# Optimization experiments

Hardware: AMD Instinct MI355X
Metric: run time of the kernel (lower is better)

## Reference

```python
import jax, jax.numpy as jnp
import numpy as np

N_NODES = 20000
N_EDGES = 320000
IN_CH = 512
HID = 128
HEADS = 4
OUT_CH = 256
NEG_SLOPE = 0.2


def _gat_layer(x, edge_index, W, a_src, a_dst, bias, heads, out_ch, concat):
    """PyG GATConv (add_self_loops=True, eval mode: no dropout).
    x: [N, F_in], edge_index: [2, E] (row 0 = src, row 1 = dst).
    Returns (out, alpha) with alpha: [E+N, heads].
    """
    N = x.shape[0]
    h = (x @ W).reshape(N, heads, out_ch)                      # [N, H, C]
    loops = jnp.arange(N, dtype=edge_index.dtype)
    src = jnp.concatenate([edge_index[0], loops])
    dst = jnp.concatenate([edge_index[1], loops])
    a_s = jnp.einsum('nhc,hc->nh', h, a_src)                   # [N, H]
    a_d = jnp.einsum('nhc,hc->nh', h, a_dst)
    e = a_s[src] + a_d[dst]                                    # [E', H]
    e = jnp.where(e > 0, e, NEG_SLOPE * e)                     # LeakyReLU
    # segment softmax over incoming edges of each dst node
    emax = jax.ops.segment_max(e, dst, num_segments=N)
    ex = jnp.exp(e - emax[dst])
    denom = jax.ops.segment_sum(ex, dst, num_segments=N)
    alpha = ex / denom[dst]                                    # [E', H]
    msg = alpha[:, :, None] * h[src]                           # [E', H, C]
    out = jax.ops.segment_sum(msg, dst, num_segments=N)        # [N, H, C]
    out = out.reshape(N, heads * out_ch) if concat else out.mean(axis=1)
    return out + bias, alpha


def setup_inputs() -> dict:
    key = jax.random.key(0)
    ks = jax.random.split(key, 10)
    s = 0.05
    x = jax.random.normal(ks[0], (N_NODES, IN_CH), dtype=jnp.float32)
    edge_index = jax.random.randint(ks[1], (2, N_EDGES), 0, N_NODES, dtype=jnp.int32)
    W1 = jax.random.normal(ks[2], (IN_CH, HEADS * HID), dtype=jnp.float32) * s
    a_src1 = jax.random.normal(ks[3], (HEADS, HID), dtype=jnp.float32) * s
    a_dst1 = jax.random.normal(ks[4], (HEADS, HID), dtype=jnp.float32) * s
    b1 = jnp.zeros((HEADS * HID,), dtype=jnp.float32)
    W2 = jax.random.normal(ks[5], (HEADS * HID, OUT_CH), dtype=jnp.float32) * s
    a_src2 = jax.random.normal(ks[6], (1, OUT_CH), dtype=jnp.float32) * s
    a_dst2 = jax.random.normal(ks[7], (1, OUT_CH), dtype=jnp.float32) * s
    b2 = jnp.zeros((OUT_CH,), dtype=jnp.float32)
    return {"x": x, "edge_index": edge_index, "W1": W1, "a_src1": a_src1,
            "a_dst1": a_dst1, "b1": b1, "W2": W2, "a_src2": a_src2,
            "a_dst2": a_dst2, "b2": b2}


def reference(x, edge_index, W1, a_src1, a_dst1, b1, W2, a_src2, a_dst2, b2):
    h, alpha1 = _gat_layer(x, edge_index, W1, a_src1, a_dst1, b1, HEADS, HID, True)
    h = jax.nn.elu(h)
    # dropout inactive in eval mode
    out, alpha2 = _gat_layer(h, edge_index, W2, a_src2, a_dst2, b2, 1, OUT_CH, False)
    return out, alpha1, alpha2
```

## Files before the change

### kernel.cpp

```cpp
#include <hip/hip_runtime.h>
#include <hip/hip_bf16.h>
#include <cstdint>


#define NNODES 20000
#define NEDGES 320000
#define ETOT   340000
#define F1     512
#define F2     256
#define HEADS  4

typedef __bf16 bf16;
typedef __attribute__((ext_vector_type(8))) __bf16 bf16x8;
typedef __attribute__((ext_vector_type(4))) float f32x4;

__device__ __forceinline__ float bflo(unsigned p) { return __uint_as_float(p << 16); }
__device__ __forceinline__ float bfhi(unsigned p) { return __uint_as_float(p & 0xffff0000u); }

__device__ __forceinline__ void gload_lds16(const void* g, void* l) {
    __builtin_amdgcn_global_load_lds(
        (const __attribute__((address_space(1))) void*)g,
        (__attribute__((address_space(3))) void*)l, 16, 0, 0);
}

__global__ void deg_count(const int* __restrict__ ei, int* __restrict__ deg) {
    int e = blockIdx.x * blockDim.x + threadIdx.x;
    if (e >= ETOT) return;
    int dst = (e < NEDGES) ? ei[NEDGES + e] : (e - NEDGES);
    atomicAdd(&deg[dst], 1);
}

__global__ void scan_deg(const int* __restrict__ deg, int* __restrict__ offs,
                         int* __restrict__ cur) {
    __shared__ int sums[1024];
    const int t = threadIdx.x;
    const int PER = 20;
    int base = t * PER;
    int local[PER];
    int run = 0;
#pragma unroll
    for (int j = 0; j < PER; j++) {
        int i = base + j;
        int v = (i < NNODES) ? deg[i] : 0;
        local[j] = run;
        run += v;
    }
    sums[t] = run;
    __syncthreads();
    for (int o = 1; o < 1024; o <<= 1) {
        int v = (t >= o) ? sums[t - o] : 0;
        __syncthreads();
        sums[t] += v;
        __syncthreads();
    }
    int texcl = (t == 0) ? 0 : sums[t - 1];
#pragma unroll
    for (int j = 0; j < PER; j++) {
        int i = base + j;
        if (i < NNODES) {
            int e = texcl + local[j];
            cur[i] = e;
            offs[i] = e;
        }
    }
    if (t == 1023) offs[NNODES] = sums[1023];
}

__global__ void fill_csr(const int* __restrict__ ei, int* __restrict__ cur,
                         int* __restrict__ csr_src, int* __restrict__ csr_eid) {
    int e = blockIdx.x * blockDim.x + threadIdx.x;
    if (e >= ETOT) return;
    int src, dst;
    if (e < NEDGES) { src = ei[e]; dst = ei[NEDGES + e]; }
    else            { src = dst = e - NEDGES; }
    int p = atomicAdd(&cur[dst], 1);
    csr_src[p] = src;
    csr_eid[p] = e;
}

__global__ void swizzle_w(const float* __restrict__ W, bf16* __restrict__ Wh,
                          bf16* __restrict__ Wl, int K, int N) {
    int idx = blockIdx.x * blockDim.x + threadIdx.x;
    int total = (K * N) >> 3;
    if (idx >= total) return;
    int lane = idx & 63;
    int tile = idx >> 6;
    int NT = N >> 4;
    int kt = tile / NT, nt = tile - kt * NT;
    int krow = kt * 32 + (lane >> 4) * 8;
    int col  = nt * 16 + (lane & 15);
    union { bf16 b[8]; uint4 u; } hi, lo;
#pragma unroll
    for (int j = 0; j < 8; j++) {
        float w = W[(size_t)(krow + j) * N + col];
        bf16 h = (bf16)w;
        hi.b[j] = h;
        lo.b[j] = (bf16)(w - (float)h);
    }
    *(uint4*)(Wh + (size_t)idx * 8) = hi.u;
    *(uint4*)(Wl + (size_t)idx * 8) = lo.u;
}

template <int K, int N>
__global__ __launch_bounds__(256) void gemm_fused(const float* __restrict__ A,
                                                  const bf16* __restrict__ Bh,
                                                  const bf16* __restrict__ Bl,
                                                  bf16* __restrict__ Cb,
                                                  const float* __restrict__ asrc,
                                                  const float* __restrict__ adst,
                                                  float* __restrict__ as_out,
                                                  float* __restrict__ ad_out, int M) {
    __shared__ __align__(16) char smem[2][16384];
    const int lane = threadIdx.x & 63;
    const int wave = threadIdx.x >> 6;
    const int row_base = blockIdx.x * 64 + wave * 16;
    const int colt0 = blockIdx.y * 8;
    constexpr int NT = N / 16;

    const char* hbase = (const char*)Bh + (size_t)colt0 * 1024;
    const char* lbase = (const char*)Bl + (size_t)colt0 * 1024;
    auto stage = [&](int kt, int buf) {
        size_t kb = (size_t)kt * NT * 1024;
#pragma unroll
        for (int q = 0; q < 4; q++) {
            int off = wave * 4096 + q * 1024;
            const char* src = (off < 8192) ? (hbase + kb + off)
                                           : (lbase + kb + (off - 8192));
            gload_lds16(src + lane * 16, &smem[buf][off]);
        }
    };

    int arow = row_base + (lane & 15);
    if (arow >= M) arow = M - 1;
    const float* aptr = A + (size_t)arow * K + ((lane >> 4) * 8);

    f32x4 acc[8] = {};
    stage(0, 0);
    __syncthreads();
    for (int kt = 0; kt < K / 32; ++kt) {
        if (kt + 1 < K / 32) stage(kt + 1, (kt + 1) & 1);
        float av[8];
        *(float4*)(av)     = *(const float4*)(aptr + kt * 32);
        *(float4*)(av + 4) = *(const float4*)(aptr + kt * 32 + 4);
        bf16x8 ah, al;
#pragma unroll
        for (int j = 0; j < 8; j++) {
            bf16 h = (bf16)av[j];
            ah[j] = h;
            al[j] = (bf16)(av[j] - (float)h);
        }
        const char* bb = smem[kt & 1];
#pragma unroll
        for (int c = 0; c < 8; c++) {
            bf16x8 bh = *(const bf16x8*)(bb + c * 1024 + lane * 16);
            bf16x8 bl = *(const bf16x8*)(bb + 8192 + c * 1024 + lane * 16);
            acc[c] = __builtin_amdgcn_mfma_f32_16x16x32_bf16(ah, bh, acc[c], 0, 0, 0);
            acc[c] = __builtin_amdgcn_mfma_f32_16x16x32_bf16(ah, bl, acc[c], 0, 0, 0);
            acc[c] = __builtin_amdgcn_mfma_f32_16x16x32_bf16(al, bh, acc[c], 0, 0, 0);
        }
        __syncthreads();
    }

    const int crow0 = row_base + (lane >> 4) * 4;
    const int col15 = lane & 15;
#pragma unroll
    for (int c = 0; c < 8; c++)
#pragma unroll
        for (int r = 0; r < 4; r++) {
            int rr = crow0 + r;
            if (rr < M)
                Cb[(size_t)rr * N + (colt0 + c) * 16 + col15] = (bf16)acc[c][r];
        }

    float ss[4] = {}, sd[4] = {};
#pragma unroll
    for (int c = 0; c < 8; c++) {
        int cw = blockIdx.y * 128 + c * 16 + col15;
        float was = asrc[cw];
        float wad = adst[cw];
#pragma unroll
        for (int r = 0; r < 4; r++) {
            ss[r] += acc[c][r] * was;
            sd[r] += acc[c][r] * wad;
        }
    }
#pragma unroll
    for (int o = 1; o < 16; o <<= 1)
#pragma unroll
        for (int r = 0; r < 4; r++) {
            ss[r] += __shfl_xor(ss[r], o);
            sd[r] += __shfl_xor(sd[r], o);
        }
    if (col15 == 0) {
        if constexpr (N == 512) {
#pragma unroll
            for (int r = 0; r < 4; r++) {
                int rr = crow0 + r;
                if (rr < M) {
                    as_out[rr * 4 + blockIdx.y] = ss[r];
                    ad_out[rr * 4 + blockIdx.y] = sd[r];
                }
            }
        } else {
#pragma unroll
            for (int r = 0; r < 4; r++) {
                int rr = crow0 + r;
                if (rr < M) {
                    atomicAdd(&as_out[rr], ss[r]);
                    atomicAdd(&ad_out[rr], sd[r]);
                }
            }
        }
    }
}

__global__ __launch_bounds__(64) void agg1(const bf16* __restrict__ h1b,
                                           const float* __restrict__ as1,
                                           const float* __restrict__ ad1,
                                           const int* __restrict__ offs,
                                           const int* __restrict__ csr_src,
                                           const int* __restrict__ csr_eid,
                                           const float* __restrict__ b1,
                                           float* __restrict__ alpha1,
                                           float* __restrict__ h1e) {
    const int n = blockIdx.x;
    const int lane = threadIdx.x;
    const int beg = offs[n];
    const int deg = offs[n + 1] - beg;

    __shared__ int   s_src[64];
    __shared__ float s_al[64][4];

    float4 ad4 = *(const float4*)(ad1 + n * 4);
    const float adn[4] = {ad4.x, ad4.y, ad4.z, ad4.w};

    float v0[4];
    int s0 = 0, e0 = 0;
    float mx[4] = {-3e38f, -3e38f, -3e38f, -3e38f};
    for (int idx = lane; idx < deg; idx += 64) {
        int s = csr_src[beg + idx];
        float4 a4 = *(const float4*)(as1 + s * 4);
        float v[4] = {a4.x + adn[0], a4.y + adn[1], a4.z + adn[2], a4.w + adn[3]};
#pragma unroll
        for (int h = 0; h < 4; h++) {
            v[h] = v[h] > 0.f ? v[h] : 0.2f * v[h];
            mx[h] = fmaxf(mx[h], v[h]);
        }
        if (idx == lane) {
            s0 = s; e0 = csr_eid[beg + idx];
#pragma unroll
            for (int h = 0; h < 4; h++) v0[h] = v[h];
        }
    }
#pragma unroll
    for (int o = 1; o < 64; o <<= 1)
#pragma unroll
        for (int h = 0; h < 4; h++) mx[h] = fmaxf(mx[h], __shfl_xor(mx[h], o));

    float ex0[4] = {0.f, 0.f, 0.f, 0.f};
    float ls[4] = {0.f, 0.f, 0.f, 0.f};
    if (lane < deg) {
#pragma unroll
        for (int h = 0; h < 4; h++) { ex0[h] = __expf(v0[h] - mx[h]); ls[h] = ex0[h]; }
    }
    for (int idx = lane + 64; idx < deg; idx += 64) {
        int s = csr_src[beg + idx];
        float4 a4 = *(const float4*)(as1 + s * 4);
        float v[4] = {a4.x + adn[0], a4.y + adn[1], a4.z + adn[2], a4.w + adn[3]};
#pragma unroll
        for (int h = 0; h < 4; h++) {
            v[h] = v[h] > 0.f ? v[h] : 0.2f * v[h];
            ls[h] += __expf(v[h] - mx[h]);
        }
    }
#pragma unroll
    for (int o = 1; o < 64; o <<= 1)
#pragma unroll
        for (int h = 0; h < 4; h++) ls[h] += __shfl_xor(ls[h], o);
    float rden[4];
#pragma unroll
    for (int h = 0; h < 4; h++) rden[h] = 1.f / ls[h];

    float acc[8] = {};
    const int myh = lane >> 4;
    for (int base = 0; base < deg; base += 64) {
        int idx = base + lane;
        if (idx < deg) {
            int s, e;
            float al[4];
            if (base == 0) {
                s = s0; e = e0;
#pragma unroll
                for (int h = 0; h < 4; h++) al[h] = ex0[h] * rden[h];
            } else {
                s = csr_src[beg + idx];
                e = csr_eid[beg + idx];
                float4 a4 = *(const float4*)(as1 + s * 4);
                float v[4] = {a4.x + adn[0], a4.y + adn[1], a4.z + adn[2], a4.w + adn[3]};
#pragma unroll
                for (int h = 0; h < 4; h++) {
                    v[h] = v[h] > 0.f ? v[h] : 0.2f * v[h];
                    al[h] = __expf(v[h] - mx[h]) * rden[h];
                }
            }
            s_src[lane] = s;
#pragma unroll
            for (int h = 0; h < 4; h++) s_al[lane][h] = al[h];
            *(float4*)(alpha1 + (size_t)e * 4) = make_float4(al[0], al[1], al[2], al[3]);
        }
        __syncthreads();
        int cnt = min(64, deg - base);
        for (int i = 0; i < cnt; i++) {
            int s = s_src[i];
            float a = s_al[i][myh];
            uint4 p = *(const uint4*)(h1b + (size_t)s * F1 + lane * 8);
            acc[0] += a * bflo(p.x); acc[1] += a * bfhi(p.x);
            acc[2] += a * bflo(p.y); acc[3] += a * bfhi(p.y);
            acc[4] += a * bflo(p.z); acc[5] += a * bfhi(p.z);
            acc[6] += a * bflo(p.w); acc[7] += a * bfhi(p.w);
        }
        __syncthreads();
    }
    const int c8 = lane * 8;
    float bv[8];
    *(float4*)(bv)     = *(const float4*)(b1 + c8);
    *(float4*)(bv + 4) = *(const float4*)(b1 + c8 + 4);
    float o[8];
#pragma unroll
    for (int j = 0; j < 8; j++) {
        float t = acc[j] + bv[j];
        o[j] = t > 0.f ? t : expm1f(t);
    }
    *(float4*)(h1e + (size_t)n * F1 + c8)     = make_float4(o[0], o[1], o[2], o[3]);
    *(float4*)(h1e + (size_t)n * F1 + c8 + 4) = make_float4(o[4], o[5], o[6], o[7]);
}

__global__ __launch_bounds__(64) void agg2(const bf16* __restrict__ h2b,
                                           const float* __restrict__ as2,
                                           const float* __restrict__ ad2,
                                           const int* __restrict__ offs,
                                           const int* __restrict__ csr_src,
                                           const int* __restrict__ csr_eid,
                                           const float* __restrict__ b2,
                                           float* __restrict__ alpha2,
                                           float* __restrict__ out) {
    const int n = blockIdx.x;
    const int lane = threadIdx.x;
    const int beg = offs[n];
    const int deg = offs[n + 1] - beg;

    __shared__ int   s_src[64];
    __shared__ float s_al[64];

    const float adn = ad2[n];

    float v0 = 0.f;
    int s0 = 0, e0 = 0;
    float mx = -3e38f;
    for (int idx = lane; idx < deg; idx += 64) {
        int s = csr_src[beg + idx];
        float v = as2[s] + adn;
        v = v > 0.f ? v : 0.2f * v;
        mx = fmaxf(mx, v);
        if (idx == lane) { s0 = s; e0 = csr_eid[beg + idx]; v0 = v; }
    }
#pragma unroll
    for (int o = 1; o < 64; o <<= 1) mx = fmaxf(mx, __shfl_xor(mx, o));

    float ex0 = 0.f, ls = 0.f;
    if (lane < deg) { ex0 = __expf(v0 - mx); ls = ex0; }
    for (int idx = lane + 64; idx < deg; idx += 64) {
        int s = csr_src[beg + idx];
        float v = as2[s] + adn;
        v = v > 0.f ? v : 0.2f * v;
        ls += __expf(v - mx);
    }
#pragma unroll
    for (int o = 1; o < 64; o <<= 1) ls += __shfl_xor(ls, o);
    float rden = 1.f / ls;

    float acc[4] = {};
    for (int base = 0; base < deg; base += 64) {
        int idx = base + lane;
        if (idx < deg) {
            int s, e;
            float a;
            if (base == 0) { s = s0; e = e0; a = ex0 * rden; }
            else {
                s = csr_src[beg + idx];
                e = csr_eid[beg + idx];
                float v = as2[s] + adn;
                v = v > 0.f ? v : 0.2f * v;
                a = __expf(v - mx) * rden;
            }
            s_src[lane] = s;
            s_al[lane] = a;
            alpha2[e] = a;
        }
        __syncthreads();
        int cnt = min(64, deg - base);
        for (int i = 0; i < cnt; i++) {
            int s = s_src[i];
            float a = s_al[i];
            uint2 p = *(const uint2*)(h2b + (size_t)s * F2 + lane * 4);
            acc[0] += a * bflo(p.x); acc[1] += a * bfhi(p.x);
            acc[2] += a * bflo(p.y); acc[3] += a * bfhi(p.y);
        }
        __syncthreads();
    }
    const int c4 = lane * 4;
    float4 bv = *(const float4*)(b2 + c4);
    *(float4*)(out + (size_t)n * F2 + c4) =
        make_float4(acc[0] + bv.x, acc[1] + bv.y, acc[2] + bv.z, acc[3] + bv.w);
}

extern "C" void kernel_launch(void* const* d_in, const int* in_sizes, int n_in,
                              void* d_out, int out_size, void* d_ws, size_t ws_size,
                              hipStream_t stream) {
    const float* x      = (const float*)d_in[0];
    const int*   ei     = (const int*)d_in[1];
    const float* W1     = (const float*)d_in[2];
    const float* a_src1 = (const float*)d_in[3];
    const float* a_dst1 = (const float*)d_in[4];
    const float* b1     = (const float*)d_in[5];
    const float* W2     = (const float*)d_in[6];
    const float* a_src2 = (const float*)d_in[7];
    const float* a_dst2 = (const float*)d_in[8];
    const float* b2     = (const float*)d_in[9];

    char* ws = (char*)d_ws;
    size_t off = 0;
    auto alloc = [&](size_t bytes) -> char* {
        char* p = ws + off;
        off += (bytes + 255) & ~(size_t)255;
        return p;
    };
    bf16*  h1b  = (bf16*) alloc((size_t)NNODES * F1 * 2);
    bf16*  h2b  = (bf16*) alloc((size_t)NNODES * F2 * 2);
    float* h1e  = (float*)alloc((size_t)NNODES * F1 * 4);
    float* as1  = (float*)alloc((size_t)NNODES * 4 * 4);
    float* ad1  = (float*)alloc((size_t)NNODES * 4 * 4);
    float* as2  = (float*)alloc((size_t)NNODES * 4);
    float* ad2  = (float*)alloc((size_t)NNODES * 4);
    bf16*  W1h  = (bf16*) alloc((size_t)512 * 512 * 2);
    bf16*  W1l  = (bf16*) alloc((size_t)512 * 512 * 2);
    bf16*  W2h  = (bf16*) alloc((size_t)512 * 256 * 2);
    bf16*  W2l  = (bf16*) alloc((size_t)512 * 256 * 2);
    int*   deg  = (int*)  alloc((size_t)NNODES * 4);
    int*   offs = (int*)  alloc((size_t)(NNODES + 1) * 4);
    int*   cur  = (int*)  alloc((size_t)NNODES * 4);
    int*   csrS = (int*)  alloc((size_t)ETOT * 4);
    int*   csrE = (int*)  alloc((size_t)ETOT * 4);

    float* out2   = (float*)d_out;
    float* alpha1 = out2 + (size_t)NNODES * F2;
    float* alpha2 = alpha1 + (size_t)ETOT * HEADS;

    hipMemsetAsync(deg, 0, (size_t)NNODES * 4, stream);
    hipMemsetAsync(as2, 0, (size_t)NNODES * 4, stream);
    hipMemsetAsync(ad2, 0, (size_t)NNODES * 4, stream);
    deg_count<<<(ETOT + 255) / 256, 256, 0, stream>>>(ei, deg);
    scan_deg<<<1, 1024, 0, stream>>>(deg, offs, cur);
    fill_csr<<<(ETOT + 255) / 256, 256, 0, stream>>>(ei, cur, csrS, csrE);

    swizzle_w<<<(512 * 512 / 8 + 255) / 256, 256, 0, stream>>>(W1, W1h, W1l, 512, 512);
    swizzle_w<<<(512 * 256 / 8 + 255) / 256, 256, 0, stream>>>(W2, W2h, W2l, 512, 256);

    gemm_fused<512, 512><<<dim3(313, 4), 256, 0, stream>>>(
        x, W1h, W1l, h1b, a_src1, a_dst1, as1, ad1, NNODES);
    agg1<<<NNODES, 64, 0, stream>>>(h1b, as1, ad1, offs, csrS, csrE, b1, alpha1, h1e);

    gemm_fused<512, 256><<<dim3(313, 2), 256, 0, stream>>>(
        h1e, W2h, W2l, h2b, a_src2, a_dst2, as2, ad2, NNODES);
    agg2<<<NNODES, 64, 0, stream>>>(h2b, as2, ad2, offs, csrS, csrE, b2, alpha2, out2);
}
```

Baseline: 324.8 us.

## Retile GEMM rows, split aggregation across channel blocks, pre-split layer-2 input to bf16

The first GEMM now gives each wave two 16-row tiles, so every B tile loaded into LDS feeds twice as many MFMAs, and A loads are prefetched one k-step ahead. The aggregation kernels split each node's channels across 8 or 4 blocks and broadcast edge weights by wave shuffles instead of LDS and barriers. agg1 writes the ELU output as a bf16 hi/lo pair, so the second GEMM reads prepared operands instead of fp32. The two weight swizzles and three memsets are also merged into one launch each. The channel split repeats the softmax work once per channel block and makes scalar bf16 gathers, and the extra row tile raises register pressure.

```diff
diff --git a/kernel.cpp b/kernel.cpp
--- a/kernel.cpp
+++ b/kernel.cpp
@@ -13,9 +13,6 @@
 typedef __bf16 bf16;
 typedef __attribute__((ext_vector_type(8))) __bf16 bf16x8;
 typedef __attribute__((ext_vector_type(4))) float f32x4;
-
-__device__ __forceinline__ float bflo(unsigned p) { return __uint_as_float(p << 16); }
-__device__ __forceinline__ float bfhi(unsigned p) { return __uint_as_float(p & 0xffff0000u); }
 
 __device__ __forceinline__ void gload_lds16(const void* g, void* l) {
     __builtin_amdgcn_global_load_lds(
@@ -78,11 +75,8 @@
     csr_eid[p] = e;
 }
 
-__global__ void swizzle_w(const float* __restrict__ W, bf16* __restrict__ Wh,
-                          bf16* __restrict__ Wl, int K, int N) {
-    int idx = blockIdx.x * blockDim.x + threadIdx.x;
-    int total = (K * N) >> 3;
-    if (idx >= total) return;
+__device__ __forceinline__ void swz(const float* __restrict__ W, bf16* __restrict__ Wh,
+                                    bf16* __restrict__ Wl, int N, int idx) {
     int lane = idx & 63;
     int tile = idx >> 6;
     int NT = N >> 4;
@@ -101,8 +95,20 @@
     *(uint4*)(Wl + (size_t)idx * 8) = lo.u;
 }
 
-template <int K, int N>
+__global__ void swizzle_both(const float* __restrict__ W1, bf16* __restrict__ W1h,
+                             bf16* __restrict__ W1l, const float* __restrict__ W2,
+                             bf16* __restrict__ W2h, bf16* __restrict__ W2l) {
+    int idx = blockIdx.x * blockDim.x + threadIdx.x;
+    const int t1 = (512 * 512) >> 3;
+    const int t2 = (512 * 256) >> 3;
+    if (idx < t1) swz(W1, W1h, W1l, 512, idx);
+    else if (idx < t1 + t2) swz(W2, W2h, W2l, 256, idx - t1);
+}
+
+template <int K, int N, int RT, bool ASPLIT>
 __global__ __launch_bounds__(256) void gemm_fused(const float* __restrict__ A,
+                                                  const bf16* __restrict__ Ah,
+                                                  const bf16* __restrict__ Al,
                                                   const bf16* __restrict__ Bh,
                                                   const bf16* __restrict__ Bl,
                                                   bf16* __restrict__ Cb,
@@ -113,7 +119,7 @@
     __shared__ __align__(16) char smem[2][16384];
     const int lane = threadIdx.x & 63;
     const int wave = threadIdx.x >> 6;
-    const int row_base = blockIdx.x * 64 + wave * 16;
+    const int row_base = blockIdx.x * (4 * RT * 16) + wave * (RT * 16);
     const int colt0 = blockIdx.y * 8;
     constexpr int NT = N / 16;
 
@@ -130,87 +136,132 @@
         }
     };
 
-    int arow = row_base + (lane & 15);
-    if (arow >= M) arow = M - 1;
-    const float* aptr = A + (size_t)arow * K + ((lane >> 4) * 8);
-
-    f32x4 acc[8] = {};
+    const float* aptr[RT];
+    const bf16 *ahp[RT], *alp[RT];
+#pragma unroll
+    for (int t = 0; t < RT; t++) {
+        int r = row_base + t * 16 + (lane & 15);
+        if (r >= M) r = M - 1;
+        if constexpr (ASPLIT) {
+            ahp[t] = Ah + (size_t)r * K + ((lane >> 4) * 8);
+            alp[t] = Al + (size_t)r * K + ((lane >> 4) * 8);
+        } else {
+            aptr[t] = A + (size_t)r * K + ((lane >> 4) * 8);
+        }
+    }
+
+    float4 nf[RT][2];
+    bf16x8 nah[RT], nal[RT];
+    auto fetchA = [&](int kt) {
+#pragma unroll
+        for (int t = 0; t < RT; t++) {
+            if constexpr (ASPLIT) {
+                nah[t] = *(const bf16x8*)(ahp[t] + kt * 32);
+                nal[t] = *(const bf16x8*)(alp[t] + kt * 32);
+            } else {
+                nf[t][0] = *(const float4*)(aptr[t] + kt * 32);
+                nf[t][1] = *(const float4*)(aptr[t] + kt * 32 + 4);
+            }
+        }
+    };
+    bf16x8 cah[RT], cal[RT];
+    auto cvtA = [&]() {
+#pragma unroll
+        for (int t = 0; t < RT; t++) {
+            if constexpr (ASPLIT) {
+                cah[t] = nah[t];
+                cal[t] = nal[t];
+            } else {
+                float av[8];
+                *(float4*)(av)     = nf[t][0];
+                *(float4*)(av + 4) = nf[t][1];
+#pragma unroll
+                for (int j = 0; j < 8; j++) {
+                    bf16 h = (bf16)av[j];
+                    cah[t][j] = h;
+                    cal[t][j] = (bf16)(av[j] - (float)h);
+                }
+            }
+        }
+    };
+
+    f32x4 acc[RT][8] = {};
     stage(0, 0);
+    fetchA(0);
     __syncthreads();
     for (int kt = 0; kt < K / 32; ++kt) {
-        if (kt + 1 < K / 32) stage(kt + 1, (kt + 1) & 1);
-        float av[8];
-        *(float4*)(av)     = *(const float4*)(aptr + kt * 32);
-        *(float4*)(av + 4) = *(const float4*)(aptr + kt * 32 + 4);
-        bf16x8 ah, al;
-#pragma unroll
-        for (int j = 0; j < 8; j++) {
-            bf16 h = (bf16)av[j];
-            ah[j] = h;
-            al[j] = (bf16)(av[j] - (float)h);
+        cvtA();
+        if (kt + 1 < K / 32) {
+            stage(kt + 1, (kt + 1) & 1);
+            fetchA(kt + 1);
         }
         const char* bb = smem[kt & 1];
 #pragma unroll
         for (int c = 0; c < 8; c++) {
             bf16x8 bh = *(const bf16x8*)(bb + c * 1024 + lane * 16);
             bf16x8 bl = *(const bf16x8*)(bb + 8192 + c * 1024 + lane * 16);
-            acc[c] = __builtin_amdgcn_mfma_f32_16x16x32_bf16(ah, bh, acc[c], 0, 0, 0);
-            acc[c] = __builtin_amdgcn_mfma_f32_16x16x32_bf16(ah, bl, acc[c], 0, 0, 0);
-            acc[c] = __builtin_amdgcn_mfma_f32_16x16x32_bf16(al, bh, acc[c], 0, 0, 0);
+#pragma unroll
+            for (int t = 0; t < RT; t++) {
+                acc[t][c] = __builtin_amdgcn_mfma_f32_16x16x32_bf16(cah[t], bh, acc[t][c], 0, 0, 0);
+                acc[t][c] = __builtin_amdgcn_mfma_f32_16x16x32_bf16(cah[t], bl, acc[t][c], 0, 0, 0);
+                acc[t][c] = __builtin_amdgcn_mfma_f32_16x16x32_bf16(cal[t], bh, acc[t][c], 0, 0, 0);
+            }
         }
         __syncthreads();
     }
 
-    const int crow0 = row_base + (lane >> 4) * 4;
+    const int qrow = (lane >> 4) * 4;
     const int col15 = lane & 15;
 #pragma unroll
-    for (int c = 0; c < 8; c++)
-#pragma unroll
-        for (int r = 0; r < 4; r++) {
-            int rr = crow0 + r;
-            if (rr < M)
-                Cb[(size_t)rr * N + (colt0 + c) * 16 + col15] = (bf16)acc[c][r];
-        }
-
-    float ss[4] = {}, sd[4] = {};
+    for (int t = 0; t < RT; t++)
+#pragma unroll
+        for (int c = 0; c < 8; c++)
+#pragma unroll
+            for (int r = 0; r < 4; r++) {
+                int rr = row_base + t * 16 + qrow + r;
+                if (rr < M)
+                    Cb[(size_t)rr * N + (colt0 + c) * 16 + col15] = (bf16)acc[t][c][r];
+            }
+
+    float ss[RT][4] = {}, sd[RT][4] = {};
 #pragma unroll
     for (int c = 0; c < 8; c++) {
         int cw = blockIdx.y * 128 + c * 16 + col15;
         float was = asrc[cw];
         float wad = adst[cw];
 #pragma unroll
-        for (int r = 0; r < 4; r++) {
-            ss[r] += acc[c][r] * was;
-            sd[r] += acc[c][r] * wad;
-        }
+        for (int t = 0; t < RT; t++)
+#pragma unroll
+            for (int r = 0; r < 4; r++) {
+                ss[t][r] += acc[t][c][r] * was;
+                sd[t][r] += acc[t][c][r] * wad;
+            }
     }
 #pragma unroll
     for (int o = 1; o < 16; o <<= 1)
 #pragma unroll
-        for (int r = 0; r < 4; r++) {
-            ss[r] += __shfl_xor(ss[r], o);
-            sd[r] += __shfl_xor(sd[r], o);
-        }
+        for (int t = 0; t < RT; t++)
+#pragma unroll
+            for (int r = 0; r < 4; r++) {
+                ss[t][r] += __shfl_xor(ss[t][r], o);
+                sd[t][r] += __shfl_xor(sd[t][r], o);
+            }
     if (col15 == 0) {
-        if constexpr (N == 512) {
+#pragma unroll
+        for (int t = 0; t < RT; t++)
 #pragma unroll
             for (int r = 0; r < 4; r++) {
-                int rr = crow0 + r;
+                int rr = row_base + t * 16 + qrow + r;
                 if (rr < M) {
-                    as_out[rr * 4 + blockIdx.y] = ss[r];
-                    ad_out[rr * 4 + blockIdx.y] = sd[r];
+                    if constexpr (N == 512) {
+                        as_out[rr * 4 + blockIdx.y] = ss[t][r];
+                        ad_out[rr * 4 + blockIdx.y] = sd[t][r];
+                    } else {
+                        atomicAdd(&as_out[rr], ss[t][r]);
+                        atomicAdd(&ad_out[rr], sd[t][r]);
+                    }
                 }
             }
-        } else {
-#pragma unroll
-            for (int r = 0; r < 4; r++) {
-                int rr = crow0 + r;
-                if (rr < M) {
-                    atomicAdd(&as_out[rr], ss[r]);
-                    atomicAdd(&ad_out[rr], sd[r]);
-                }
-            }
-        }
     }
 }
 
@@ -218,139 +269,124 @@
                                            const float* __restrict__ as1,
                                            const float* __restrict__ ad1,
                                            const int* __restrict__ offs,
-                                           const int* __restrict__ csr_src,
-                                           const int* __restrict__ csr_eid,
+                                           const int* __restrict__ csrS,
+                                           const int* __restrict__ csrE,
                                            const float* __restrict__ b1,
                                            float* __restrict__ alpha1,
-                                           float* __restrict__ h1e) {
-    const int n = blockIdx.x;
+                                           bf16* __restrict__ h1eh,
+                                           bf16* __restrict__ h1el) {
+    const int n = blockIdx.x >> 3, cq = blockIdx.x & 7;
     const int lane = threadIdx.x;
+    const int h = cq >> 1;
     const int beg = offs[n];
     const int deg = offs[n + 1] - beg;
 
-    __shared__ int   s_src[64];
-    __shared__ float s_al[64][4];
-
     float4 ad4 = *(const float4*)(ad1 + n * 4);
     const float adn[4] = {ad4.x, ad4.y, ad4.z, ad4.w};
 
-    float v0[4];
+    float v0[4] = {};
     int s0 = 0, e0 = 0;
     float mx[4] = {-3e38f, -3e38f, -3e38f, -3e38f};
     for (int idx = lane; idx < deg; idx += 64) {
-        int s = csr_src[beg + idx];
+        int s = csrS[beg + idx];
         float4 a4 = *(const float4*)(as1 + s * 4);
         float v[4] = {a4.x + adn[0], a4.y + adn[1], a4.z + adn[2], a4.w + adn[3]};
 #pragma unroll
-        for (int h = 0; h < 4; h++) {
-            v[h] = v[h] > 0.f ? v[h] : 0.2f * v[h];
-            mx[h] = fmaxf(mx[h], v[h]);
+        for (int k = 0; k < 4; k++) {
+            v[k] = v[k] > 0.f ? v[k] : 0.2f * v[k];
+            mx[k] = fmaxf(mx[k], v[k]);
         }
         if (idx == lane) {
-            s0 = s; e0 = csr_eid[beg + idx];
-#pragma unroll
-            for (int h = 0; h < 4; h++) v0[h] = v[h];
+            s0 = s; e0 = csrE[beg + idx];
+#pragma unroll
+            for (int k = 0; k < 4; k++) v0[k] = v[k];
         }
     }
 #pragma unroll
     for (int o = 1; o < 64; o <<= 1)
 #pragma unroll
-        for (int h = 0; h < 4; h++) mx[h] = fmaxf(mx[h], __shfl_xor(mx[h], o));
+        for (int k = 0; k < 4; k++) mx[k] = fmaxf(mx[k], __shfl_xor(mx[k], o));
 
     float ex0[4] = {0.f, 0.f, 0.f, 0.f};
     float ls[4] = {0.f, 0.f, 0.f, 0.f};
     if (lane < deg) {
 #pragma unroll
-        for (int h = 0; h < 4; h++) { ex0[h] = __expf(v0[h] - mx[h]); ls[h] = ex0[h]; }
+        for (int k = 0; k < 4; k++) { ex0[k] = __expf(v0[k] - mx[k]); ls[k] = ex0[k]; }
     }
     for (int idx = lane + 64; idx < deg; idx += 64) {
-        int s = csr_src[beg + idx];
+        int s = csrS[beg + idx];
         float4 a4 = *(const float4*)(as1 + s * 4);
         float v[4] = {a4.x + adn[0], a4.y + adn[1], a4.z + adn[2], a4.w + adn[3]};
 #pragma unroll
-        for (int h = 0; h < 4; h++) {
-            v[h] = v[h] > 0.f ? v[h] : 0.2f * v[h];
-            ls[h] += __expf(v[h] - mx[h]);
+        for (int k = 0; k < 4; k++) {
+            v[k] = v[k] > 0.f ? v[k] : 0.2f * v[k];
+            ls[k] += __expf(v[k] - mx[k]);
         }
     }
 #pragma unroll
     for (int o = 1; o < 64; o <<= 1)
 #pragma unroll
-        for (int h = 0; h < 4; h++) ls[h] += __shfl_xor(ls[h], o);
+        for (int k = 0; k < 4; k++) ls[k] += __shfl_xor(ls[k], o);
     float rden[4];
 #pragma unroll
-    for (int h = 0; h < 4; h++) rden[h] = 1.f / ls[h];
-
-    float acc[8] = {};
-    const int myh = lane >> 4;
+    for (int k = 0; k < 4; k++) rden[k] = 1.f / ls[k];
+
+    float acc = 0.f;
+    const int ch = (cq << 6) + lane;
     for (int base = 0; base < deg; base += 64) {
         int idx = base + lane;
+        int cnt = min(64, deg - base);
+        float myal = 0.f;
+        int mys = 0;
         if (idx < deg) {
+            float al[4];
             int s, e;
-            float al[4];
             if (base == 0) {
                 s = s0; e = e0;
 #pragma unroll
-                for (int h = 0; h < 4; h++) al[h] = ex0[h] * rden[h];
+                for (int k = 0; k < 4; k++) al[k] = ex0[k] * rden[k];
             } else {
-                s = csr_src[beg + idx];
-                e = csr_eid[beg + idx];
+                s = csrS[beg + idx];
+                e = csrE[beg + idx];
                 float4 a4 = *(const float4*)(as1 + s * 4);
                 float v[4] = {a4.x + adn[0], a4.y + adn[1], a4.z + adn[2], a4.w + adn[3]};
 #pragma unroll
-                for (int h = 0; h < 4; h++) {
-                    v[h] = v[h] > 0.f ? v[h] : 0.2f * v[h];
-                    al[h] = __expf(v[h] - mx[h]) * rden[h];
+                for (int k = 0; k < 4; k++) {
+                    v[k] = v[k] > 0.f ? v[k] : 0.2f * v[k];
+                    al[k] = __expf(v[k] - mx[k]) * rden[k];
                 }
             }
-            s_src[lane] = s;
-#pragma unroll
-            for (int h = 0; h < 4; h++) s_al[lane][h] = al[h];
-            *(float4*)(alpha1 + (size_t)e * 4) = make_float4(al[0], al[1], al[2], al[3]);
-        }
-        __syncthreads();
-        int cnt = min(64, deg - base);
+            mys = s;
+            myal = al[h];
+            if (cq == 0)
+                *(float4*)(alpha1 + (size_t)e * 4) = make_float4(al[0], al[1], al[2], al[3]);
+        }
         for (int i = 0; i < cnt; i++) {
-            int s = s_src[i];
-            float a = s_al[i][myh];
-            uint4 p = *(const uint4*)(h1b + (size_t)s * F1 + lane * 8);
-            acc[0] += a * bflo(p.x); acc[1] += a * bfhi(p.x);
-            acc[2] += a * bflo(p.y); acc[3] += a * bfhi(p.y);
-            acc[4] += a * bflo(p.z); acc[5] += a * bfhi(p.z);
-            acc[6] += a * bflo(p.w); acc[7] += a * bfhi(p.w);
-        }
-        __syncthreads();
-    }
-    const int c8 = lane * 8;
-    float bv[8];
-    *(float4*)(bv)     = *(const float4*)(b1 + c8);
-    *(float4*)(bv + 4) = *(const float4*)(b1 + c8 + 4);
-    float o[8];
-#pragma unroll
-    for (int j = 0; j < 8; j++) {
-        float t = acc[j] + bv[j];
-        o[j] = t > 0.f ? t : expm1f(t);
-    }
-    *(float4*)(h1e + (size_t)n * F1 + c8)     = make_float4(o[0], o[1], o[2], o[3]);
-    *(float4*)(h1e + (size_t)n * F1 + c8 + 4) = make_float4(o[4], o[5], o[6], o[7]);
+            int s = __shfl(mys, i);
+            float a = __shfl(myal, i);
+            acc += a * (float)h1b[(size_t)s * F1 + ch];
+        }
+    }
+    float t = acc + b1[ch];
+    t = t > 0.f ? t : expm1f(t);
+    bf16 hi = (bf16)t;
+    h1eh[(size_t)n * F1 + ch] = hi;
+    h1el[(size_t)n * F1 + ch] = (bf16)(t - (float)hi);
 }
 
 __global__ __launch_bounds__(64) void agg2(const bf16* __restrict__ h2b,
                                            const float* __restrict__ as2,
                                            const float* __restrict__ ad2,
                                            const int* __restrict__ offs,
-                                           const int* __restrict__ csr_src,
-                                           const int* __restrict__ csr_eid,
+                                           const int* __restrict__ csrS,
+                                           const int* __restrict__ csrE,
                                            const float* __restrict__ b2,
                                            float* __restrict__ alpha2,
                                            float* __restrict__ out) {
-    const int n = blockIdx.x;
+    const int n = blockIdx.x >> 2, cq = blockIdx.x & 3;
     const int lane = threadIdx.x;
     const int beg = offs[n];
     const int deg = offs[n + 1] - beg;
-
-    __shared__ int   s_src[64];
-    __shared__ float s_al[64];
 
     const float adn = ad2[n];
 
@@ -358,11 +394,11 @@
     int s0 = 0, e0 = 0;
     float mx = -3e38f;
     for (int idx = lane; idx < deg; idx += 64) {
-        int s = csr_src[beg + idx];
+        int s = csrS[beg + idx];
         float v = as2[s] + adn;
         v = v > 0.f ? v : 0.2f * v;
         mx = fmaxf(mx, v);
-        if (idx == lane) { s0 = s; e0 = csr_eid[beg + idx]; v0 = v; }
+        if (idx == lane) { s0 = s; e0 = csrE[beg + idx]; v0 = v; }
     }
 #pragma unroll
     for (int o = 1; o < 64; o <<= 1) mx = fmaxf(mx, __shfl_xor(mx, o));
@@ -370,7 +406,7 @@
     float ex0 = 0.f, ls = 0.f;
     if (lane < deg) { ex0 = __expf(v0 - mx); ls = ex0; }
     for (int idx = lane + 64; idx < deg; idx += 64) {
-        int s = csr_src[beg + idx];
+        int s = csrS[beg + idx];
         float v = as2[s] + adn;
         v = v > 0.f ? v : 0.2f * v;
         ls += __expf(v - mx);
@@ -379,39 +415,35 @@
     for (int o = 1; o < 64; o <<= 1) ls += __shfl_xor(ls, o);
     float rden = 1.f / ls;
 
-    float acc[4] = {};
+    float acc = 0.f;
+    const int ch = (cq << 6) + lane;
     for (int base = 0; base < deg; base += 64) {
         int idx = base + lane;
+        int cnt = min(64, deg - base);
+        float myal = 0.f;
+        int mys = 0;
         if (idx < deg) {
+            float a;
             int s, e;
-            float a;
             if (base == 0) { s = s0; e = e0; a = ex0 * rden; }
             else {
-                s = csr_src[beg + idx];
-                e = csr_eid[beg + idx];
+                s = csrS[beg + idx];
+                e = csrE[beg + idx];
                 float v = as2[s] + adn;
                 v = v > 0.f ? v : 0.2f * v;
                 a = __expf(v - mx) * rden;
             }
-            s_src[lane] = s;
-            s_al[lane] = a;
-            alpha2[e] = a;
-        }
-        __syncthreads();
-        int cnt = min(64, deg - base);
+            mys = s;
+            myal = a;
+            if (cq == 0) alpha2[e] = a;
+        }
         for (int i = 0; i < cnt; i++) {
-            int s = s_src[i];
-            float a = s_al[i];
-            uint2 p = *(const uint2*)(h2b + (size_t)s * F2 + lane * 4);
-            acc[0] += a * bflo(p.x); acc[1] += a * bfhi(p.x);
-            acc[2] += a * bflo(p.y); acc[3] += a * bfhi(p.y);
-        }
-        __syncthreads();
-    }
-    const int c4 = lane * 4;
-    float4 bv = *(const float4*)(b2 + c4);
-    *(float4*)(out + (size_t)n * F2 + c4) =
-        make_float4(acc[0] + bv.x, acc[1] + bv.y, acc[2] + bv.z, acc[3] + bv.w);
+            int s = __shfl(mys, i);
+            float a = __shfl(myal, i);
+            acc += a * (float)h2b[(size_t)s * F2 + ch];
+        }
+    }
+    out[(size_t)n * F2 + ch] = acc + b2[ch];
 }
 
 extern "C" void kernel_launch(void* const* d_in, const int* in_sizes, int n_in,
@@ -437,16 +469,17 @@
     };
     bf16*  h1b  = (bf16*) alloc((size_t)NNODES * F1 * 2);
     bf16*  h2b  = (bf16*) alloc((size_t)NNODES * F2 * 2);
-    float* h1e  = (float*)alloc((size_t)NNODES * F1 * 4);
+    bf16*  h1eh = (bf16*) alloc((size_t)NNODES * F1 * 2);
+    bf16*  h1el = (bf16*) alloc((size_t)NNODES * F1 * 2);
     float* as1  = (float*)alloc((size_t)NNODES * 4 * 4);
     float* ad1  = (float*)alloc((size_t)NNODES * 4 * 4);
+    int*   deg  = (int*)  alloc((size_t)NNODES * 4);
     float* as2  = (float*)alloc((size_t)NNODES * 4);
     float* ad2  = (float*)alloc((size_t)NNODES * 4);
     bf16*  W1h  = (bf16*) alloc((size_t)512 * 512 * 2);
     bf16*  W1l  = (bf16*) alloc((size_t)512 * 512 * 2);
     bf16*  W2h  = (bf16*) alloc((size_t)512 * 256 * 2);
     bf16*  W2l  = (bf16*) alloc((size_t)512 * 256 * 2);
-    int*   deg  = (int*)  alloc((size_t)NNODES * 4);
     int*   offs = (int*)  alloc((size_t)(NNODES + 1) * 4);
     int*   cur  = (int*)  alloc((size_t)NNODES * 4);
     int*   csrS = (int*)  alloc((size_t)ETOT * 4);
@@ -456,21 +489,20 @@
     float* alpha1 = out2 + (size_t)NNODES * F2;
     float* alpha2 = alpha1 + (size_t)ETOT * HEADS;
 
-    hipMemsetAsync(deg, 0, (size_t)NNODES * 4, stream);
-    hipMemsetAsync(as2, 0, (size_t)NNODES * 4, stream);
-    hipMemsetAsync(ad2, 0, (size_t)NNODES * 4, stream);
+    hipMemsetAsync(deg, 0, (size_t)((char*)ad2 - (char*)deg) + NNODES * 4, stream);
     deg_count<<<(ETOT + 255) / 256, 256, 0, stream>>>(ei, deg);
     scan_deg<<<1, 1024, 0, stream>>>(deg, offs, cur);
     fill_csr<<<(ETOT + 255) / 256, 256, 0, stream>>>(ei, cur, csrS, csrE);
 
-    swizzle_w<<<(512 * 512 / 8 + 255) / 256, 256, 0, stream>>>(W1, W1h, W1l, 512, 512);
-    swizzle_w<<<(512 * 256 / 8 + 255) / 256, 256, 0, stream>>>(W2, W2h, W2l, 512, 256);
-
-    gemm_fused<512, 512><<<dim3(313, 4), 256, 0, stream>>>(
-        x, W1h, W1l, h1b, a_src1, a_dst1, as1, ad1, NNODES);
-    agg1<<<NNODES, 64, 0, stream>>>(h1b, as1, ad1, offs, csrS, csrE, b1, alpha1, h1e);
-
-    gemm_fused<512, 256><<<dim3(313, 2), 256, 0, stream>>>(
-        h1e, W2h, W2l, h2b, a_src2, a_dst2, as2, ad2, NNODES);
-    agg2<<<NNODES, 64, 0, stream>>>(h2b, as2, ad2, offs, csrS, csrE, b2, alpha2, out2);
-}
+    swizzle_both<<<(49152 + 255) / 256, 256, 0, stream>>>(W1, W1h, W1l, W2, W2h, W2l);
+
+    gemm_fused<512, 512, 2, false><<<dim3(157, 4), 256, 0, stream>>>(
+        x, nullptr, nullptr, W1h, W1l, h1b, a_src1, a_dst1, as1, ad1, NNODES);
+    agg1<<<NNODES * 8, 64, 0, stream>>>(h1b, as1, ad1, offs, csrS, csrE, b1,
+                                        alpha1, h1eh, h1el);
+
+    gemm_fused<512, 256, 1, true><<<dim3(313, 2), 256, 0, stream>>>(
+        nullptr, h1eh, h1el, W2h, W2l, h2b, a_src2, a_dst2, as2, ad2, NNODES);
+    agg2<<<NNODES * 4, 64, 0, stream>>>(h2b, as2, ad2, offs, csrS, csrE, b2,
+                                        alpha2, out2);
+}
```

Measured after the change: 489.5 us. 50.7% more time.
